# Kernel tuning notes

Measured on AMD Instinct MI355X. Metric: run time of the kernel, lower is better.

The kernel has to match this reference:

```python
import jax, jax.numpy as jnp
import numpy as np

N = 256

def _dct_mat(n):
    # orthonormal DCT-II matrix: (D @ v) == scipy.fftpack.dct(v, norm='ortho')
    k = np.arange(n)[:, None]
    i = np.arange(n)[None, :]
    D = np.cos(np.pi * (2 * i + 1) * k / (2 * n)) * np.sqrt(2.0 / n)
    D[0] *= np.sqrt(0.5)
    return jnp.asarray(D, jnp.float32)

DCT = _dct_mat(N)

def conv3(x, w, b):
    y = jax.lax.conv_general_dilated(x, w, (1, 1), [(1, 1), (1, 1)],
                                     dimension_numbers=('NCHW', 'OIHW', 'NCHW'))
    return y + b[None, :, None, None]

def bn(x, g, b, m, v):
    inv = jax.lax.rsqrt(v + 1e-5)
    return (x - m[None, :, None, None]) * (inv * g)[None, :, None, None] + b[None, :, None, None]

def pool2(x):
    B, C, H, W = x.shape
    return x.reshape(B, C, H // 2, 2, W // 2, 2).mean(axis=(3, 5))


def setup_inputs() -> dict:
    key = jax.random.key(0)
    ks = jax.random.split(key, 32)
    B = 16
    d = {}
    d['x'] = jax.random.normal(ks[0], (B, 3, N, N), jnp.float32)
    d['dct_mean'] = jax.random.normal(ks[1], (3, N, N), jnp.float32) * 0.1
    d['dct_std'] = jnp.abs(jax.random.normal(ks[2], (3, N, N), jnp.float32)) + 0.5
    d['w_spa'] = jax.random.normal(ks[3], (32, 3, 3, 3), jnp.float32) * 0.1
    d['b_spa'] = jnp.zeros((32,), jnp.float32)
    d['w_fre'] = jax.random.normal(ks[4], (32, 3, 3, 3), jnp.float32) * 0.1
    d['b_fre'] = jnp.zeros((32,), jnp.float32)
    d['bn0_g'] = jnp.abs(jax.random.normal(ks[5], (64,), jnp.float32)) + 0.5
    d['bn0_b'] = jax.random.normal(ks[6], (64,), jnp.float32) * 0.1
    d['bn0_m'] = jax.random.normal(ks[7], (64,), jnp.float32) * 0.1
    d['bn0_v'] = jax.random.uniform(ks[8], (64,), jnp.float32) + 0.5
    d['cls_w1'] = jax.random.normal(ks[9], (32, 64, 3, 3), jnp.float32) * 0.05
    d['cls_b1'] = jnp.zeros((32,), jnp.float32)
    d['cls_w'] = jax.random.normal(ks[10], (9, 32, 32, 3, 3), jnp.float32) * 0.05
    d['cls_b'] = jnp.zeros((9, 32), jnp.float32)
    d['cbn_g'] = jnp.abs(jax.random.normal(ks[11], (10, 32), jnp.float32)) + 0.5
    d['cbn_b'] = jax.random.normal(ks[12], (10, 32), jnp.float32) * 0.1
    d['cbn_m'] = jax.random.normal(ks[13], (10, 32), jnp.float32) * 0.1
    d['cbn_v'] = jax.random.uniform(ks[14], (10, 32), jnp.float32) + 0.5
    d['fc_w'] = jax.random.normal(ks[15], (2, 32), jnp.float32) * 0.1
    d['fc_b'] = jnp.zeros((2,), jnp.float32)
    return d


def reference(x, dct_mean, dct_std, w_spa, b_spa, w_fre, b_fre,
              bn0_g, bn0_b, bn0_m, bn0_v,
              cls_w1, cls_b1, cls_w, cls_b,
              cbn_g, cbn_b, cbn_m, cbn_v, fc_w, fc_b):
    # DCT branch: torch code detaches x before DCT
    xd = jax.lax.stop_gradient(x)
    # dct2: DCT along last axis then second-to-last -> D @ X @ D^T
    xf = jnp.einsum('ij,bcjk,lk->bcil', DCT, xd, DCT)
    xf = jnp.log(jnp.abs(xf) + 1e-13)
    xf = (xf - dct_mean[None]) / dct_std[None]

    fs = conv3(x, w_spa, b_spa)
    ff = conv3(xf, w_fre, b_fre)
    feat = jnp.concatenate([fs, ff], axis=1)  # [B,64,256,256]
    feature_map = jax.nn.relu(bn(feat, bn0_g, bn0_b, bn0_m, bn0_v))

    # classifier: 10 conv-BN-ReLU layers, avg-pool after layers 4, 6, 8
    h = jax.nn.relu(bn(conv3(feature_map, cls_w1, cls_b1),
                       cbn_g[0], cbn_b[0], cbn_m[0], cbn_v[0]))
    for i in range(9):  # layers 2..10
        h = jax.nn.relu(bn(conv3(h, cls_w[i], cls_b[i]),
                           cbn_g[i + 1], cbn_b[i + 1], cbn_m[i + 1], cbn_v[i + 1]))
        if i in (2, 4, 6):  # after overall layer 4, 6, 8
            h = pool2(h)
    h = h.mean(axis=(2, 3))  # adaptive avg pool to 1x1 + flatten -> [B,32]
    logits = h @ fc_w.T + fc_b
    return logits, feature_map
```

## Files before the change

kernel.cpp:

```cpp
#include <hip/hip_runtime.h>
#include <hip/hip_bf16.h>
#include <math.h>

typedef __hip_bfloat16 bf16;
typedef __attribute__((ext_vector_type(8))) short short8;
typedef __attribute__((ext_vector_type(4))) float f32x4;

__device__ __forceinline__ float b2f(short s) {
  unsigned u = ((unsigned)(unsigned short)s) << 16;
  return __builtin_bit_cast(float, u);
}
__device__ __forceinline__ short f2b(float f) {
  bf16 h = __float2bfloat16(f);
  return *reinterpret_cast<short*>(&h);
}

__global__ void k_build_dct(float* __restrict__ D) {
  int k = blockIdx.x, i = threadIdx.x;
  double v = cos(3.14159265358979323846 * (2.0 * i + 1.0) * (double)k / 512.0) *
             0.08838834764831845;
  if (k == 0) v *= 0.7071067811865476;
  D[k * 256 + i] = (float)v;
}

__global__ void k_pack_w(const float* __restrict__ w1,
                         const float* __restrict__ wc, short* __restrict__ wp) {
  int set = blockIdx.x;
  const float* w;
  int C, cbase;
  if (set < 2) {
    w = w1;
    C = 64;
    cbase = set * 32;
  } else {
    w = wc + (set - 2) * 9216;
    C = 32;
    cbase = 0;
  }
  for (int d = threadIdx.x; d < 9216; d += 256) {
    int k = d & 7, l = (d >> 3) & 63, ct = (d >> 9) & 1, tap = d >> 10;
    int co = ct * 16 + (l & 15), cin = (l >> 4) * 8 + k;
    wp[set * 9216 + d] = f2b(w[(co * C + cbase + cin) * 9 + tap]);
  }
}

__global__ __launch_bounds__(256) void k_dct1(const float* __restrict__ D,
                                              const float* __restrict__ x,
                                              float* __restrict__ M1) {
  __shared__ __align__(16) float As[32][84];
  __shared__ __align__(16) float Bs[32][80];
  int tid = threadIdx.x;
  int tx = tid & 15, ty = tid >> 4;
  int k0 = blockIdx.x * 64, i0 = blockIdx.y * 64;
  size_t base = (size_t)blockIdx.z * 65536;
  float acc[4][4];
#pragma unroll
  for (int a = 0; a < 4; ++a)
#pragma unroll
    for (int c = 0; c < 4; ++c) acc[a][c] = 0.f;
  for (int kk = 0; kk < 256; kk += 32) {
    __syncthreads();
#pragma unroll
    for (int s = 0; s < 2; ++s) {
      int idx = s * 256 + tid;
      int i = idx >> 3, k4 = (idx & 7) * 4;
      f32x4 d4 = *(const f32x4*)&D[(i0 + i) * 256 + kk + k4];
#pragma unroll
      for (int q = 0; q < 4; ++q) As[k4 + q][i] = d4[q];
      int j = idx >> 4, c4 = (idx & 15) * 4;
      *(f32x4*)&Bs[j][c4] =
          *(const f32x4*)&x[base + (size_t)(kk + j) * 256 + k0 + c4];
    }
    __syncthreads();
#pragma unroll
    for (int k = 0; k < 32; ++k) {
      f32x4 a4 = *(const f32x4*)&As[k][ty * 4];
      f32x4 b4 = *(const f32x4*)&Bs[k][tx * 4];
#pragma unroll
      for (int ii = 0; ii < 4; ++ii)
#pragma unroll
        for (int jj = 0; jj < 4; ++jj)
          acc[ii][jj] = fmaf(a4[ii], b4[jj], acc[ii][jj]);
    }
  }
#pragma unroll
  for (int ii = 0; ii < 4; ++ii) {
    f32x4 o = {acc[ii][0], acc[ii][1], acc[ii][2], acc[ii][3]};
    *(f32x4*)&M1[base + (size_t)(i0 + ty * 4 + ii) * 256 + k0 + tx * 4] = o;
  }
}

__global__ __launch_bounds__(256) void k_dct2(const float* __restrict__ M1,
                                              const float* __restrict__ D,
                                              const float* __restrict__ dmean,
                                              const float* __restrict__ dstd,
                                              float* __restrict__ xf) {
  __shared__ __align__(16) float As[32][84];
  __shared__ __align__(16) float Bs[32][84];
  int tid = threadIdx.x;
  int tx = tid & 15, ty = tid >> 4;
  int l0 = blockIdx.x * 64, i0 = blockIdx.y * 64;
  int bc = blockIdx.z;
  size_t base = (size_t)bc * 65536;
  int ch = bc % 3;
  float acc[4][4];
#pragma unroll
  for (int a = 0; a < 4; ++a)
#pragma unroll
    for (int c = 0; c < 4; ++c) acc[a][c] = 0.f;
  for (int kk = 0; kk < 256; kk += 32) {
    __syncthreads();
#pragma unroll
    for (int s = 0; s < 2; ++s) {
      int idx = s * 256 + tid;
      int i = idx >> 3, k4 = (idx & 7) * 4;
      f32x4 a4 = *(const f32x4*)&M1[base + (size_t)(i0 + i) * 256 + kk + k4];
      f32x4 b4 = *(const f32x4*)&D[(l0 + i) * 256 + kk + k4];
#pragma unroll
      for (int q = 0; q < 4; ++q) {
        As[k4 + q][i] = a4[q];
        Bs[k4 + q][i] = b4[q];
      }
    }
    __syncthreads();
#pragma unroll
    for (int k = 0; k < 32; ++k) {
      f32x4 a4 = *(const f32x4*)&As[k][ty * 4];
      f32x4 b4 = *(const f32x4*)&Bs[k][tx * 4];
#pragma unroll
      for (int ii = 0; ii < 4; ++ii)
#pragma unroll
        for (int jj = 0; jj < 4; ++jj)
          acc[ii][jj] = fmaf(a4[ii], b4[jj], acc[ii][jj]);
    }
  }
#pragma unroll
  for (int ii = 0; ii < 4; ++ii) {
    int ig = i0 + ty * 4 + ii;
    int ll = l0 + tx * 4;
    int mi = (ch * 256 + ig) * 256 + ll;
    f32x4 dm = *(const f32x4*)&dmean[mi];
    f32x4 ds = *(const f32x4*)&dstd[mi];
    f32x4 o;
#pragma unroll
    for (int jj = 0; jj < 4; ++jj)
      o[jj] = (logf(fabsf(acc[ii][jj]) + 1e-13f) - dm[jj]) / ds[jj];
    *(f32x4*)&xf[base + (size_t)ig * 256 + ll] = o;
  }
}

__global__ __launch_bounds__(256) void k_front_n(
    const float* __restrict__ x, const float* __restrict__ xf,
    const float* __restrict__ w_spa, const float* __restrict__ b_spa,
    const float* __restrict__ w_fre, const float* __restrict__ b_fre,
    const float* __restrict__ g, const float* __restrict__ bb,
    const float* __restrict__ m, const float* __restrict__ vv,
    short* __restrict__ featN0, short* __restrict__ featN1,
    float* __restrict__ feat) {
  __shared__ __align__(16) float xin[3 * 4 * 264];
  __shared__ __align__(16) short fstage[2 * 256 * 32];
  __shared__ float wl[864];
  __shared__ float sc[32], sh[32];
  int z = blockIdx.z;
  const float* in = z ? xf : x;
  const float* w = z ? w_fre : w_spa;
  const float* bias = z ? b_fre : b_spa;
  int tid = threadIdx.x;
  int b = blockIdx.y;
  int y0 = blockIdx.x * 2;
  for (int i = tid; i < 864; i += 256) wl[i] = w[i];
  if (tid < 32) {
    int cgl = z * 32 + tid;
    float s = g[cgl] * rsqrtf(vv[cgl] + 1e-5f);
    sc[tid] = s;
    sh[tid] = (bias[tid] - m[cgl]) * s + bb[cgl];
  }
  const float* inb = in + (size_t)b * 3 * 65536;
  for (int i = tid; i < 792; i += 256) {
    int ci = i / 264, rem = i - ci * 264;
    int r = rem / 66, c = rem - r * 66;
    int gy = y0 - 1 + r;
    f32x4 v = {0.f, 0.f, 0.f, 0.f};
    if ((unsigned)gy < 256u && c >= 1 && c <= 64)
      v = *(const f32x4*)&inb[((size_t)ci << 16) + (gy << 8) + (c * 4 - 4)];
    *(f32x4*)&xin[(ci * 4 + r) * 264 + c * 4] = v;
  }
  __syncthreads();
  int xq = tid & 63, cg = tid >> 6;
  int x0 = xq * 4;
  float acc[2][4][8];
#pragma unroll
  for (int r = 0; r < 2; ++r)
#pragma unroll
    for (int p = 0; p < 4; ++p)
#pragma unroll
      for (int co = 0; co < 8; ++co) acc[r][p][co] = 0.f;
  for (int ci = 0; ci < 3; ++ci) {
    float v[4][6];
#pragma unroll
    for (int r = 0; r < 4; ++r) {
      const float* row = &xin[(ci * 4 + r) * 264];
      f32x4 qA = *(const f32x4*)&row[x0];
      f32x4 qB = *(const f32x4*)&row[x0 + 4];
      f32x4 qC = *(const f32x4*)&row[x0 + 8];
      v[r][0] = qA[3];
      v[r][1] = qB[0];
      v[r][2] = qB[1];
      v[r][3] = qB[2];
      v[r][4] = qB[3];
      v[r][5] = qC[0];
    }
#pragma unroll
    for (int co = 0; co < 8; ++co) {
      int cob = cg * 8 + co;
      float w9[9];
#pragma unroll
      for (int t = 0; t < 9; ++t) w9[t] = wl[cob * 27 + ci * 9 + t];
#pragma unroll
      for (int ky = 0; ky < 3; ++ky)
#pragma unroll
        for (int kx = 0; kx < 3; ++kx) {
          float wv = w9[ky * 3 + kx];
#pragma unroll
          for (int r = 0; r < 2; ++r)
#pragma unroll
            for (int p = 0; p < 4; ++p)
              acc[r][p][co] = fmaf(v[r + ky][p + kx], wv, acc[r][p][co]);
        }
    }
  }
#pragma unroll
  for (int r = 0; r < 2; ++r) {
#pragma unroll
    for (int p = 0; p < 4; ++p) {
      short8 s8;
#pragma unroll
      for (int co = 0; co < 8; ++co) {
        float val = acc[r][p][co] * sc[cg * 8 + co] + sh[cg * 8 + co];
        val = val > 0.f ? val : 0.f;
        acc[r][p][co] = val;
        s8[co] = f2b(val);
      }
      int scg = cg ^ p ^ (xq & 3);
      *(short8*)&fstage[((r * 256 + x0 + p) << 5) + (scg << 3)] = s8;
    }
#pragma unroll
    for (int co = 0; co < 8; ++co) {
      f32x4 o = {acc[r][0][co], acc[r][1][co], acc[r][2][co], acc[r][3][co]};
      f32x4* dst = (f32x4*)&feat[(((size_t)(b * 64 + z * 32 + cg * 8 + co))
                                  << 16) +
                                 ((y0 + r) << 8) + x0];
      __builtin_nontemporal_store(o, dst);
    }
  }
  __syncthreads();
  short* fp = z ? featN1 : featN0;
  size_t rowbase = ((size_t)(b * 256 + y0) * 256) << 5;
#pragma unroll
  for (int k = 0; k < 8; ++k) {
    int c = k * 256 + tid;
    int p2 = (c >> 2) & 255;
    int r = c >> 10;
    int cgc = c & 3;
    int scg = cgc ^ (p2 & 3) ^ ((p2 >> 2) & 3);
    short8 v = *(short8*)&fstage[((r * 256 + p2) << 5) + (scg << 3)];
    *(short8*)(fp + rowbase + (size_t)c * 8) = v;
  }
}

template <int TX, int NP, int YB, bool POOL, bool GW>
__global__ __launch_bounds__(256) void k_conv4(
    const short* __restrict__ in0, const short* __restrict__ in1,
    const float* __restrict__ w, const short* __restrict__ wp,
    const float* __restrict__ bias, const float* __restrict__ g,
    const float* __restrict__ bb, const float* __restrict__ m,
    const float* __restrict__ vv, short* __restrict__ out, int H) {
  constexpr int XT = TX + 2;
  constexpr int NR = (TX == 64) ? YB : 2;
  constexpr int YR = ((TX == 64) ? YB : 4) + 2;
  __shared__ short tile[YR * XT * 32];
  __shared__ short wlds[GW ? 1 : 9216];
  __shared__ float sc[32], sh[32];
  int tid = threadIdx.x;
  int lane = tid & 63, wid = tid >> 6;
  int W = H;
  int b = blockIdx.z, y0 = blockIdx.y * ((TX == 64) ? YB : 4),
      x0 = blockIdx.x * TX;
  if (tid < 32) {
    float s = g[tid] * rsqrtf(vv[tid] + 1e-5f);
    sc[tid] = s;
    sh[tid] = (bias[tid] - m[tid]) * s + bb[tid];
  }
  int px = lane & 15, g4 = lane >> 4;
  int RB = (TX == 64) ? 0 : (wid >> 1) * 2;
  int wx = (TX == 64) ? wid : (wid & 1);
  f32x4 acc[NR][2];
#pragma unroll
  for (int r = 0; r < NR; ++r)
#pragma unroll
    for (int ct = 0; ct < 2; ++ct) acc[r][ct] = {0.f, 0.f, 0.f, 0.f};

  for (int cb = 0; cb < NP; ++cb) {
    if (cb) __syncthreads();
    if constexpr (!GW) {
      for (int d = tid; d < 9216; d += 256) {
        int k = d & 7, l = (d >> 3) & 63, ct = (d >> 9) & 1, tap = d >> 10;
        int co = ct * 16 + (l & 15), cin = (l >> 4) * 8 + k;
        wlds[d] = f2b(w[(co * (NP * 32) + cb * 32 + cin) * 9 + tap]);
      }
    }
    const short* in = cb ? in1 : in0;
    for (int i = tid; i < YR * XT * 4; i += 256) {
      int ir = i / (XT * 4), rem = i - ir * (XT * 4);
      int xl = rem >> 2, cg = rem & 3;
      int gy = y0 - 1 + ir, gx = x0 - 1 + xl;
      short8 v = {0, 0, 0, 0, 0, 0, 0, 0};
      if ((unsigned)gy < (unsigned)H && (unsigned)gx < (unsigned)W)
        v = *(const short8*)(in + (((size_t)(b * H + gy) * W + gx) << 5) + cg * 8);
      *(short8*)&tile[(ir * XT + xl) * 32 +
                      ((cg ^ (xl & 3) ^ ((xl >> 2) & 3)) << 3)] = v;
    }
    __syncthreads();
    short8 wf[9][2];
#pragma unroll
    for (int tap = 0; tap < 9; ++tap)
#pragma unroll
      for (int ct = 0; ct < 2; ++ct) {
        if constexpr (GW)
          wf[tap][ct] = *(const short8*)(wp + cb * 9216 +
                                         ((((tap * 2 + ct) << 6) + lane) << 3));
        else
          wf[tap][ct] = *(short8*)&wlds[(((tap * 2 + ct) << 6) + lane) << 3];
      }
#pragma unroll
    for (int dx = 0; dx < 3; ++dx) {
      int xl = wx * 16 + px + dx;
      int cs = (g4 ^ (xl & 3) ^ ((xl >> 2) & 3)) << 3;
      short8 fr[NR + 2];
#pragma unroll
      for (int ir = 0; ir < NR + 2; ++ir)
        fr[ir] = *(short8*)&tile[((RB + ir) * XT + xl) * 32 + cs];
#pragma unroll
      for (int dy = 0; dy < 3; ++dy)
#pragma unroll
        for (int r = 0; r < NR; ++r)
#pragma unroll
          for (int ct = 0; ct < 2; ++ct)
            acc[r][ct] = __builtin_amdgcn_mfma_f32_16x16x32_bf16(
                wf[dy * 3 + dx][ct], fr[r + dy], acc[r][ct], 0, 0, 0);
    }
  }
  int xg = x0 + wx * 16 + px;
  if constexpr (POOL) {
    int H2 = H >> 1;
#pragma unroll
    for (int pr = 0; pr < NR / 2; ++pr) {
#pragma unroll
      for (int ct = 0; ct < 2; ++ct) {
        unsigned short u[4];
#pragma unroll
        for (int q = 0; q < 4; ++q) {
          int co = ct * 16 + g4 * 4 + q;
          float v0 = acc[2 * pr][ct][q] * sc[co] + sh[co];
          float v1 = acc[2 * pr + 1][ct][q] * sc[co] + sh[co];
          v0 = v0 > 0.f ? v0 : 0.f;
          v1 = v1 > 0.f ? v1 : 0.f;
          float s2 = v0 + v1;
          float o = s2 + __shfl_xor(s2, 1, 64);
          u[q] = (unsigned short)f2b(0.25f * o);
        }
        if (!(px & 1)) {
          uint2 pk;
          pk.x = (unsigned)u[0] | ((unsigned)u[1] << 16);
          pk.y = (unsigned)u[2] | ((unsigned)u[3] << 16);
          int row = (y0 + RB + 2 * pr) >> 1;
          size_t ob = (((size_t)(b * H2 + row) * H2 + (xg >> 1)) << 5) +
                      ct * 16 + g4 * 4;
          *(uint2*)(out + ob) = pk;
        }
      }
    }
  } else {
#pragma unroll
    for (int r = 0; r < NR; ++r) {
      int y = y0 + RB + r;
      size_t ob = (((size_t)(b * H + y) * W + xg) << 5);
#pragma unroll
      for (int ct = 0; ct < 2; ++ct) {
        unsigned short u[4];
#pragma unroll
        for (int q = 0; q < 4; ++q) {
          int co = ct * 16 + g4 * 4 + q;
          float val = acc[r][ct][q] * sc[co] + sh[co];
          val = val > 0.f ? val : 0.f;
          u[q] = (unsigned short)f2b(val);
        }
        uint2 pk;
        pk.x = (unsigned)u[0] | ((unsigned)u[1] << 16);
        pk.y = (unsigned)u[2] | ((unsigned)u[3] << 16);
        *(uint2*)(out + ob + ct * 16 + g4 * 4) = pk;
      }
    }
  }
}

__global__ __launch_bounds__(256) void k_conv_front(
    const float* __restrict__ x, const float* __restrict__ xf,
    const float* __restrict__ w_spa, const float* __restrict__ b_spa,
    const float* __restrict__ w_fre, const float* __restrict__ b_fre,
    const float* __restrict__ g, const float* __restrict__ bb,
    const float* __restrict__ m, const float* __restrict__ vv,
    float* __restrict__ feat) {
  int z = blockIdx.z;
  const float* in = z ? xf : x;
  const float* w = z ? w_fre : w_spa;
  const float* bias = z ? b_fre : b_spa;
  __shared__ float wl[864];
  __shared__ float sc[32], sh[32];
  int tid = threadIdx.x;
  for (int i = tid; i < 864; i += 256) wl[i] = w[i];
  if (tid < 32) {
    int cg = z * 32 + tid;
    float s = g[cg] * rsqrtf(vv[cg] + 1e-5f);
    sc[tid] = s;
    sh[tid] = (bias[tid] - m[cg]) * s + bb[cg];
  }
  __syncthreads();
  int b = blockIdx.y;
  int idx = blockIdx.x * 256 + tid;
  int ry = idx >> 8;
  int xx = idx & 255;
  int y0 = ry * 2;
  const float* inb = in + (size_t)b * 3 * 65536;
  float a0[32], a1[32];
#pragma unroll
  for (int co = 0; co < 32; ++co) {
    a0[co] = 0.f;
    a1[co] = 0.f;
  }
  for (int ci = 0; ci < 3; ++ci) {
    const float* p = inb + (size_t)ci * 65536;
    float v[4][3];
#pragma unroll
    for (int r = 0; r < 4; ++r) {
      int iy = y0 + r - 1;
      bool yok = (unsigned)iy < 256u;
#pragma unroll
      for (int c = 0; c < 3; ++c) {
        int ix = xx + c - 1;
        v[r][c] = (yok && (unsigned)ix < 256u) ? p[iy * 256 + ix] : 0.f;
      }
    }
#pragma unroll
    for (int t9 = 0; t9 < 9; ++t9) {
      int ky = t9 / 3, kx = t9 % 3;
      float v0 = v[ky][kx], v1 = v[ky + 1][kx];
#pragma unroll
      for (int co = 0; co < 32; ++co) {
        float wv = wl[co * 27 + ci * 9 + t9];
        a0[co] = fmaf(v0, wv, a0[co]);
        a1[co] = fmaf(v1, wv, a1[co]);
      }
    }
  }
#pragma unroll
  for (int co = 0; co < 32; ++co) {
    size_t o = ((size_t)(b * 64 + z * 32 + co) * 256 + y0) * 256 + xx;
    float r0 = a0[co] * sc[co] + sh[co];
    float r1 = a1[co] * sc[co] + sh[co];
    feat[o] = r0 > 0.f ? r0 : 0.f;
    feat[o + 256] = r1 > 0.f ? r1 : 0.f;
  }
}

__global__ __launch_bounds__(256) void k_conv1_mfma(
    const float* __restrict__ in, const float* __restrict__ w,
    const float* __restrict__ bias, const float* __restrict__ g,
    const float* __restrict__ bb, const float* __restrict__ m,
    const float* __restrict__ vv, short* __restrict__ out) {
  constexpr int TX = 64, XT = 66;
  __shared__ short tile[4 * XT * 64];
  __shared__ short wlds[9216];
  __shared__ float sc[32], sh[32];
  int tid = threadIdx.x;
  int lane = tid & 63, wid = tid >> 6;
  int b = blockIdx.z, y0 = blockIdx.y * 2, x0 = blockIdx.x * TX;
  if (tid < 32) {
    float s = g[tid] * rsqrtf(vv[tid] + 1e-5f);
    sc[tid] = s;
    sh[tid] = (bias[tid] - m[tid]) * s + bb[tid];
  }
  for (int ir = 0; ir < 4; ++ir) {
    int gy = y0 - 1 + ir;
    bool yok = (unsigned)gy < 256u;
    for (int ch = tid; ch < XT * 8; ch += 256) {
      int xl = ch >> 3, cg = ch & 7;
      int gx = x0 - 1 + xl;
      short8 v = {0, 0, 0, 0, 0, 0, 0, 0};
      if (yok && (unsigned)gx < 256u) {
        const float* p = in + (((size_t)(b * 64 + cg * 8)) << 16) + (gy << 8) + gx;
#pragma unroll
        for (int k = 0; k < 8; ++k) v[k] = f2b(p[(size_t)k << 16]);
      }
      *(short8*)&tile[((ir * XT + xl) << 6) + ((cg ^ (xl & 7)) << 3)] = v;
    }
  }
  int px = lane & 15, g4 = lane >> 4;
  int wx = wid;
  f32x4 acc[2][2];
#pragma unroll
  for (int r = 0; r < 2; ++r)
#pragma unroll
    for (int ct = 0; ct < 2; ++ct) acc[r][ct] = {0.f, 0.f, 0.f, 0.f};
  for (int cb = 0; cb < 2; ++cb) {
    __syncthreads();
    for (int d = tid; d < 9216; d += 256) {
      int k = d & 7, l = (d >> 3) & 63, ct = (d >> 9) & 1, tap = d >> 10;
      int co = ct * 16 + (l & 15), cin = (l >> 4) * 8 + k;
      wlds[d] = f2b(w[(co * 64 + cb * 32 + cin) * 9 + tap]);
    }
    __syncthreads();
    short8 wf[9][2];
#pragma unroll
    for (int tap = 0; tap < 9; ++tap)
#pragma unroll
      for (int ct = 0; ct < 2; ++ct)
        wf[tap][ct] = *(short8*)&wlds[(((tap * 2 + ct) << 6) + lane) << 3];
#pragma unroll
    for (int dx = 0; dx < 3; ++dx) {
      short8 fr[4];
#pragma unroll
      for (int ir = 0; ir < 4; ++ir) {
        int xl = wx * 16 + px + dx;
        fr[ir] = *(short8*)&tile[((ir * XT + xl) << 6) +
                                 (((cb * 4 + g4) ^ (xl & 7)) << 3)];
      }
#pragma unroll
      for (int dy = 0; dy < 3; ++dy)
#pragma unroll
        for (int r = 0; r < 2; ++r)
#pragma unroll
          for (int ct = 0; ct < 2; ++ct)
            acc[r][ct] = __builtin_amdgcn_mfma_f32_16x16x32_bf16(
                wf[dy * 3 + dx][ct], fr[r + dy], acc[r][ct], 0, 0, 0);
    }
  }
#pragma unroll
  for (int r = 0; r < 2; ++r) {
    int y = y0 + r;
    int xg = x0 + wx * 16 + px;
    size_t ob = (((size_t)(b * 256 + y) * 256 + xg) << 5);
#pragma unroll
    for (int ct = 0; ct < 2; ++ct) {
      unsigned short u[4];
#pragma unroll
      for (int q = 0; q < 4; ++q) {
        int co = ct * 16 + g4 * 4 + q;
        float val = acc[r][ct][q] * sc[co] + sh[co];
        val = val > 0.f ? val : 0.f;
        u[q] = (unsigned short)f2b(val);
      }
      uint2 pk;
      pk.x = (unsigned)u[0] | ((unsigned)u[1] << 16);
      pk.y = (unsigned)u[2] | ((unsigned)u[3] << 16);
      *(uint2*)(out + ob + ct * 16 + g4 * 4) = pk;
    }
  }
}

__global__ __launch_bounds__(256) void k_tail(
    const short* __restrict__ in, const float* __restrict__ w9,
    const float* __restrict__ b9, const float* __restrict__ w10,
    const float* __restrict__ b10, const float* __restrict__ cg9,
    const float* __restrict__ cb9, const float* __restrict__ cm9,
    const float* __restrict__ cv9, const float* __restrict__ cg10,
    const float* __restrict__ cb10, const float* __restrict__ cm10,
    const float* __restrict__ cv10, const float* __restrict__ fw,
    const float* __restrict__ fb, float* __restrict__ logits) {
  __shared__ short tileA[32768];
  __shared__ short tileB[32768];
  __shared__ short wlds[9216];
  __shared__ float sc[2][32], sh[2][32];
  __shared__ float red[16][8];
  __shared__ float smean[32];
  int tid = threadIdx.x;
  int lane = tid & 63, wv = tid >> 6;
  int b = blockIdx.x;
  int px = lane & 15, g4 = lane >> 4;

  if (tid < 64) {
    int l = tid >> 5, c = tid & 31;
    const float* g = l ? cg10 : cg9;
    const float* bb = l ? cb10 : cb9;
    const float* m = l ? cm10 : cm9;
    const float* v = l ? cv10 : cv9;
    const float* bi = l ? b10 : b9;
    float s = g[c] * rsqrtf(v[c] + 1e-5f);
    sc[l][c] = s;
    sh[l][c] = (bi[c] - m[c]) * s + bb[c];
  }
  const short* src = in + (size_t)b * 32768;
  for (int i = tid; i < 4096; i += 256) {
    int p = i >> 2, cg = i & 3;
    int xc = p & 31;
    short8 v = *(const short8*)(src + p * 32 + cg * 8);
    *(short8*)&tileA[p * 32 + ((cg ^ (xc & 3) ^ ((xc >> 2) & 3)) << 3)] = v;
  }
  float psum[2][4];
#pragma unroll
  for (int ct = 0; ct < 2; ++ct)
#pragma unroll
    for (int q = 0; q < 4; ++q) psum[ct][q] = 0.f;

  for (int layer = 0; layer < 2; ++layer) {
    if (layer) __syncthreads();
    const float* w = layer ? w10 : w9;
    for (int d = tid; d < 9216; d += 256) {
      int k = d & 7, l = (d >> 3) & 63, ct = (d >> 9) & 1, tap = d >> 10;
      int co = ct * 16 + (l & 15), cin = (l >> 4) * 8 + k;
      wlds[d] = f2b(w[(co * 32 + cin) * 9 + tap]);
    }
    __syncthreads();
    short8 wf[9][2];
#pragma unroll
    for (int tap = 0; tap < 9; ++tap)
#pragma unroll
      for (int ct = 0; ct < 2; ++ct)
        wf[tap][ct] = *(short8*)&wlds[(((tap * 2 + ct) << 6) + lane) << 3];
    const short* ts = layer ? tileB : tileA;
    for (int u = wv; u < 16; u += 4) {
      int rw = u >> 1, cw = u & 1;
      f32x4 acc[4][2];
#pragma unroll
      for (int r = 0; r < 4; ++r)
#pragma unroll
        for (int ct = 0; ct < 2; ++ct) acc[r][ct] = {0.f, 0.f, 0.f, 0.f};
#pragma unroll
      for (int dx = 0; dx < 3; ++dx) {
        int gx = cw * 16 + px + dx - 1;
        bool xok = (unsigned)gx < 32u;
        int cs = (g4 ^ (gx & 3) ^ ((gx >> 2) & 3)) << 3;
        short8 fr[6];
        short8 zz = {0, 0, 0, 0, 0, 0, 0, 0};
#pragma unroll
        for (int ir = 0; ir < 6; ++ir) {
          int gy = rw * 4 + ir - 1;
          fr[ir] = (xok && (unsigned)gy < 32u)
                       ? *(const short8*)&ts[(gy * 32 + gx) * 32 + cs]
                       : zz;
        }
#pragma unroll
        for (int dy = 0; dy < 3; ++dy)
#pragma unroll
          for (int r = 0; r < 4; ++r)
#pragma unroll
            for (int ct = 0; ct < 2; ++ct)
              acc[r][ct] = __builtin_amdgcn_mfma_f32_16x16x32_bf16(
                  wf[dy * 3 + dx][ct], fr[r + dy], acc[r][ct], 0, 0, 0);
      }
      int xc = cw * 16 + px;
#pragma unroll
      for (int r = 0; r < 4; ++r) {
        int y = rw * 4 + r;
#pragma unroll
        for (int ct = 0; ct < 2; ++ct) {
          float v4[4];
#pragma unroll
          for (int q = 0; q < 4; ++q) {
            int co = ct * 16 + g4 * 4 + q;
            float val = acc[r][ct][q] * sc[layer][co] + sh[layer][co];
            v4[q] = val > 0.f ? val : 0.f;
          }
          if (layer == 0) {
            int cg = ct * 2 + (g4 >> 1);
            int scg = cg ^ (xc & 3) ^ ((xc >> 2) & 3);
            uint2 pk;
            pk.x = (unsigned)(unsigned short)f2b(v4[0]) |
                   ((unsigned)(unsigned short)f2b(v4[1]) << 16);
            pk.y = (unsigned)(unsigned short)f2b(v4[2]) |
                   ((unsigned)(unsigned short)f2b(v4[3]) << 16);
            *(uint2*)&tileB[(y * 32 + xc) * 32 + (scg << 3) + (g4 & 1) * 4] = pk;
          } else {
#pragma unroll
            for (int q = 0; q < 4; ++q) psum[ct][q] += v4[q];
          }
        }
      }
    }
  }
#pragma unroll
  for (int o = 1; o < 16; o <<= 1)
#pragma unroll
    for (int ct = 0; ct < 2; ++ct)
#pragma unroll
      for (int q = 0; q < 4; ++q)
        psum[ct][q] += __shfl_xor(psum[ct][q], o, 64);
  if (px == 0) {
#pragma unroll
    for (int ct = 0; ct < 2; ++ct)
#pragma unroll
      for (int q = 0; q < 4; ++q) red[wv * 4 + g4][ct * 4 + q] = psum[ct][q];
  }
  __syncthreads();
  if (tid < 32) {
    int ct = tid >> 4, g4r = (tid >> 2) & 3, q = tid & 3;
    float s = red[g4r][ct * 4 + q] + red[4 + g4r][ct * 4 + q] +
              red[8 + g4r][ct * 4 + q] + red[12 + g4r][ct * 4 + q];
    smean[tid] = s * (1.f / 1024.f);
  }
  __syncthreads();
  if (tid < 2) {
    float s = fb[tid];
    for (int c = 0; c < 32; ++c) s = fmaf(smean[c], fw[tid * 32 + c], s);
    logits[b * 2 + tid] = s;
  }
}

extern "C" void kernel_launch(void* const* d_in, const int* in_sizes, int n_in,
                              void* d_out, int out_size, void* d_ws,
                              size_t ws_size, hipStream_t stream) {
  const float* x = (const float*)d_in[0];
  const float* dmean = (const float*)d_in[1];
  const float* dstd = (const float*)d_in[2];
  const float* w_spa = (const float*)d_in[3];
  const float* b_spa = (const float*)d_in[4];
  const float* w_fre = (const float*)d_in[5];
  const float* b_fre = (const float*)d_in[6];
  const float* bn0_g = (const float*)d_in[7];
  const float* bn0_b = (const float*)d_in[8];
  const float* bn0_m = (const float*)d_in[9];
  const float* bn0_v = (const float*)d_in[10];
  const float* cls_w1 = (const float*)d_in[11];
  const float* cls_b1 = (const float*)d_in[12];
  const float* cls_w = (const float*)d_in[13];
  const float* cls_b = (const float*)d_in[14];
  const float* cbn_g = (const float*)d_in[15];
  const float* cbn_b = (const float*)d_in[16];
  const float* cbn_m = (const float*)d_in[17];
  const float* cbn_v = (const float*)d_in[18];
  const float* fc_w = (const float*)d_in[19];
  const float* fc_b = (const float*)d_in[20];

  float* out = (float*)d_out;
  float* logits = out;
  float* feat = out + 32;

  char* ws = (char*)d_ws;
  const size_t MB = 1048576ull;
  bool bigws = ws_size >= 193ull * MB;

  short *bufA, *bufB, *featN0 = nullptr, *featN1 = nullptr, *wpack = nullptr;
  float *D, *M1, *xf;
  if (bigws) {
    featN0 = (short*)ws;
    featN1 = (short*)(ws + 64 * MB);
    bufA = (short*)(ws + 128 * MB);
    bufB = (short*)ws;
    wpack = (short*)(ws + 192 * MB);
    D = (float*)(ws + 128 * MB);
    M1 = (float*)(ws + 129 * MB);
    xf = (float*)(ws + 144 * MB);
  } else {
    bufA = (short*)ws;
    bufB = (short*)(ws + 64 * MB);
    D = (float*)ws;
    M1 = (float*)(ws + 1 * MB);
    xf = (float*)(ws + 64 * MB);
  }

  k_build_dct<<<dim3(256), dim3(256), 0, stream>>>(D);
  if (bigws) k_pack_w<<<dim3(9), dim3(256), 0, stream>>>(cls_w1, cls_w, wpack);
  k_dct1<<<dim3(4, 4, 48), dim3(256), 0, stream>>>(D, x, M1);
  k_dct2<<<dim3(4, 4, 48), dim3(256), 0, stream>>>(M1, D, dmean, dstd, xf);

  const int WS = 32 * 32 * 9;
  if (bigws) {
    k_front_n<<<dim3(128, 16, 2), dim3(256), 0, stream>>>(
        x, xf, w_spa, b_spa, w_fre, b_fre, bn0_g, bn0_b, bn0_m, bn0_v, featN0,
        featN1, feat);
    k_conv4<64, 2, 8, false, true><<<dim3(4, 32, 16), dim3(256), 0, stream>>>(
        featN0, featN1, nullptr, wpack, cls_b1, cbn_g, cbn_b, cbn_m, cbn_v,
        bufA, 256);
    k_conv4<64, 1, 8, false, true><<<dim3(4, 32, 16), dim3(256), 0, stream>>>(
        bufA, nullptr, nullptr, wpack + 2 * 9216, cls_b + 0 * 32, cbn_g + 32,
        cbn_b + 32, cbn_m + 32, cbn_v + 32, bufB, 256);
    k_conv4<64, 1, 8, false, true><<<dim3(4, 32, 16), dim3(256), 0, stream>>>(
        bufB, nullptr, nullptr, wpack + 3 * 9216, cls_b + 1 * 32, cbn_g + 64,
        cbn_b + 64, cbn_m + 64, cbn_v + 64, bufA, 256);
    k_conv4<64, 1, 8, true, true><<<dim3(4, 32, 16), dim3(256), 0, stream>>>(
        bufA, nullptr, nullptr, wpack + 4 * 9216, cls_b + 2 * 32, cbn_g + 96,
        cbn_b + 96, cbn_m + 96, cbn_v + 96, bufB, 256);
    k_conv4<64, 1, 8, false, true><<<dim3(2, 16, 16), dim3(256), 0, stream>>>(
        bufB, nullptr, nullptr, wpack + 5 * 9216, cls_b + 3 * 32, cbn_g + 128,
        cbn_b + 128, cbn_m + 128, cbn_v + 128, bufA, 128);
    k_conv4<64, 1, 8, true, true><<<dim3(2, 16, 16), dim3(256), 0, stream>>>(
        bufA, nullptr, nullptr, wpack + 6 * 9216, cls_b + 4 * 32, cbn_g + 160,
        cbn_b + 160, cbn_m + 160, cbn_v + 160, bufB, 128);
    k_conv4<32, 1, 4, false, true><<<dim3(2, 16, 16), dim3(256), 0, stream>>>(
        bufB, nullptr, nullptr, wpack + 7 * 9216, cls_b + 5 * 32, cbn_g + 192,
        cbn_b + 192, cbn_m + 192, cbn_v + 192, bufA, 64);
    k_conv4<32, 1, 4, true, true><<<dim3(2, 16, 16), dim3(256), 0, stream>>>(
        bufA, nullptr, nullptr, wpack + 8 * 9216, cls_b + 6 * 32, cbn_g + 224,
        cbn_b + 224, cbn_m + 224, cbn_v + 224, bufB, 64);
  } else {
    k_conv_front<<<dim3(128, 16, 2), dim3(256), 0, stream>>>(
        x, xf, w_spa, b_spa, w_fre, b_fre, bn0_g, bn0_b, bn0_m, bn0_v, feat);
    k_conv1_mfma<<<dim3(4, 128, 16), dim3(256), 0, stream>>>(
        feat, cls_w1, cls_b1, cbn_g, cbn_b, cbn_m, cbn_v, bufA);
    k_conv4<64, 1, 8, false, false><<<dim3(4, 32, 16), dim3(256), 0, stream>>>(
        bufA, nullptr, cls_w + 0 * WS, nullptr, cls_b + 0 * 32, cbn_g + 32,
        cbn_b + 32, cbn_m + 32, cbn_v + 32, bufB, 256);
    k_conv4<64, 1, 8, false, false><<<dim3(4, 32, 16), dim3(256), 0, stream>>>(
        bufB, nullptr, cls_w + 1 * WS, nullptr, cls_b + 1 * 32, cbn_g + 64,
        cbn_b + 64, cbn_m + 64, cbn_v + 64, bufA, 256);
    k_conv4<64, 1, 8, true, false><<<dim3(4, 32, 16), dim3(256), 0, stream>>>(
        bufA, nullptr, cls_w + 2 * WS, nullptr, cls_b + 2 * 32, cbn_g + 96,
        cbn_b + 96, cbn_m + 96, cbn_v + 96, bufB, 256);
    k_conv4<64, 1, 8, false, false><<<dim3(2, 16, 16), dim3(256), 0, stream>>>(
        bufB, nullptr, cls_w + 3 * WS, nullptr, cls_b + 3 * 32, cbn_g + 128,
        cbn_b + 128, cbn_m + 128, cbn_v + 128, bufA, 128);
    k_conv4<64, 1, 8, true, false><<<dim3(2, 16, 16), dim3(256), 0, stream>>>(
        bufA, nullptr, cls_w + 4 * WS, nullptr, cls_b + 4 * 32, cbn_g + 160,
        cbn_b + 160, cbn_m + 160, cbn_v + 160, bufB, 128);
    k_conv4<32, 1, 4, false, false><<<dim3(2, 16, 16), dim3(256), 0, stream>>>(
        bufB, nullptr, cls_w + 5 * WS, nullptr, cls_b + 5 * 32, cbn_g + 192,
        cbn_b + 192, cbn_m + 192, cbn_v + 192, bufA, 64);
    k_conv4<32, 1, 4, true, false><<<dim3(2, 16, 16), dim3(256), 0, stream>>>(
        bufA, nullptr, cls_w + 6 * WS, nullptr, cls_b + 6 * 32, cbn_g + 224,
        cbn_b + 224, cbn_m + 224, cbn_v + 224, bufB, 64);
  }

  k_tail<<<dim3(16), dim3(256), 0, stream>>>(
      bufB, cls_w + 7 * WS, cls_b + 7 * 32, cls_w + 8 * WS, cls_b + 8 * 32,
      cbn_g + 256, cbn_b + 256, cbn_m + 256, cbn_v + 256, cbn_g + 288,
      cbn_b + 288, cbn_m + 288, cbn_v + 288, fc_w, fc_b, logits);
}
```

Measured before the change: 399.1 us.

## Store intermediate classifier activations as fp8 e4m3 to halve memory traffic

Intermediate NHWC activation buffers between the conv layers are now stored as fp8 e4m3 instead of bf16. Each kernel dequantizes to bf16 when staging into shared memory, so the MFMA math is unchanged. This halves global read and write traffic for the memory-bound conv chain and shrinks the workspace layout. The cost is extra per-element conversion ALU work and reduced activation precision, which may hurt accuracy of the logits.

```diff
diff --git a/kernel.cpp b/kernel.cpp
--- a/kernel.cpp
+++ b/kernel.cpp
@@ -1,8 +1,10 @@
 #include <hip/hip_runtime.h>
 #include <hip/hip_bf16.h>
+#include <hip/hip_fp8.h>
 #include <math.h>
 
 typedef __hip_bfloat16 bf16;
+typedef unsigned char uchar;
 typedef __attribute__((ext_vector_type(8))) short short8;
 typedef __attribute__((ext_vector_type(4))) float f32x4;
 
@@ -13,6 +15,19 @@
 __device__ __forceinline__ short f2b(float f) {
   bf16 h = __float2bfloat16(f);
   return *reinterpret_cast<short*>(&h);
+}
+__device__ __forceinline__ uchar f2q(float f) {
+  __hip_fp8_e4m3 t(f);
+  return (uchar)t.__x;
+}
+__device__ __forceinline__ float q2f(uchar c) {
+  __hip_fp8_e4m3 t;
+  t.__x = (__hip_fp8_storage_t)c;
+  return (float)t;
+}
+__device__ __forceinline__ unsigned pk4q(float a, float b, float c, float d) {
+  return (unsigned)f2q(a) | ((unsigned)f2q(b) << 8) | ((unsigned)f2q(c) << 16) |
+         ((unsigned)f2q(d) << 24);
 }
 
 __global__ void k_build_dct(float* __restrict__ D) {
@@ -155,7 +170,7 @@
     const float* __restrict__ w_fre, const float* __restrict__ b_fre,
     const float* __restrict__ g, const float* __restrict__ bb,
     const float* __restrict__ m, const float* __restrict__ vv,
-    short* __restrict__ featN0, short* __restrict__ featN1,
+    uchar* __restrict__ featN0, uchar* __restrict__ featN1,
     float* __restrict__ feat) {
   __shared__ __align__(16) float xin[3 * 4 * 264];
   __shared__ __align__(16) short fstage[2 * 256 * 32];
@@ -254,8 +269,8 @@
     }
   }
   __syncthreads();
-  short* fp = z ? featN1 : featN0;
-  size_t rowbase = ((size_t)(b * 256 + y0) * 256) << 5;
+  uchar* fp = z ? featN1 : featN0;
+  size_t rowbase = ((size_t)(b * 256 + y0) * 256) * 32;
 #pragma unroll
   for (int k = 0; k < 8; ++k) {
     int c = k * 256 + tid;
@@ -264,17 +279,20 @@
     int cgc = c & 3;
     int scg = cgc ^ (p2 & 3) ^ ((p2 >> 2) & 3);
     short8 v = *(short8*)&fstage[((r * 256 + p2) << 5) + (scg << 3)];
-    *(short8*)(fp + rowbase + (size_t)c * 8) = v;
-  }
-}
-
-template <int TX, int NP, int YB, bool POOL, bool GW>
+    uint2 pk2;
+    pk2.x = pk4q(b2f(v[0]), b2f(v[1]), b2f(v[2]), b2f(v[3]));
+    pk2.y = pk4q(b2f(v[4]), b2f(v[5]), b2f(v[6]), b2f(v[7]));
+    *(uint2*)(fp + rowbase + (size_t)c * 8) = pk2;
+  }
+}
+
+template <int TX, int NP, int YB, bool POOL, bool GW, bool F8>
 __global__ __launch_bounds__(256) void k_conv4(
-    const short* __restrict__ in0, const short* __restrict__ in1,
+    const void* __restrict__ in0, const void* __restrict__ in1,
     const float* __restrict__ w, const short* __restrict__ wp,
     const float* __restrict__ bias, const float* __restrict__ g,
     const float* __restrict__ bb, const float* __restrict__ m,
-    const float* __restrict__ vv, short* __restrict__ out, int H) {
+    const float* __restrict__ vv, void* __restrict__ out, int H) {
   constexpr int XT = TX + 2;
   constexpr int NR = (TX == 64) ? YB : 2;
   constexpr int YR = ((TX == 64) ? YB : 4) + 2;
@@ -309,16 +327,41 @@
         wlds[d] = f2b(w[(co * (NP * 32) + cb * 32 + cin) * 9 + tap]);
       }
     }
-    const short* in = cb ? in1 : in0;
-    for (int i = tid; i < YR * XT * 4; i += 256) {
-      int ir = i / (XT * 4), rem = i - ir * (XT * 4);
-      int xl = rem >> 2, cg = rem & 3;
-      int gy = y0 - 1 + ir, gx = x0 - 1 + xl;
-      short8 v = {0, 0, 0, 0, 0, 0, 0, 0};
-      if ((unsigned)gy < (unsigned)H && (unsigned)gx < (unsigned)W)
-        v = *(const short8*)(in + (((size_t)(b * H + gy) * W + gx) << 5) + cg * 8);
-      *(short8*)&tile[(ir * XT + xl) * 32 +
-                      ((cg ^ (xl & 3) ^ ((xl >> 2) & 3)) << 3)] = v;
+    const void* in = cb ? in1 : in0;
+    if constexpr (F8) {
+      const uchar* inq = (const uchar*)in;
+      for (int i = tid; i < YR * XT * 2; i += 256) {
+        int ir = i / (XT * 2), rem = i - ir * (XT * 2);
+        int xl = rem >> 1, c2 = rem & 1;
+        int gy = y0 - 1 + ir, gx = x0 - 1 + xl;
+        short8 raw = {0, 0, 0, 0, 0, 0, 0, 0};
+        if ((unsigned)gy < (unsigned)H && (unsigned)gx < (unsigned)W)
+          raw = *(const short8*)(inq + ((size_t)(b * H + gy) * W + gx) * 32 +
+                                 c2 * 16);
+        const uchar* pb = (const uchar*)&raw;
+        short8 o0, o1;
+#pragma unroll
+        for (int k = 0; k < 8; ++k) {
+          o0[k] = f2b(q2f(pb[k]));
+          o1[k] = f2b(q2f(pb[k + 8]));
+        }
+        int sw = (xl & 3) ^ ((xl >> 2) & 3);
+        *(short8*)&tile[(ir * XT + xl) * 32 + (((c2 * 2) ^ sw) << 3)] = o0;
+        *(short8*)&tile[(ir * XT + xl) * 32 + (((c2 * 2 + 1) ^ sw) << 3)] = o1;
+      }
+    } else {
+      const short* ins = (const short*)in;
+      for (int i = tid; i < YR * XT * 4; i += 256) {
+        int ir = i / (XT * 4), rem = i - ir * (XT * 4);
+        int xl = rem >> 2, cg = rem & 3;
+        int gy = y0 - 1 + ir, gx = x0 - 1 + xl;
+        short8 v = {0, 0, 0, 0, 0, 0, 0, 0};
+        if ((unsigned)gy < (unsigned)H && (unsigned)gx < (unsigned)W)
+          v = *(const short8*)(ins + (((size_t)(b * H + gy) * W + gx) << 5) +
+                               cg * 8);
+        *(short8*)&tile[(ir * XT + xl) * 32 +
+                        ((cg ^ (xl & 3) ^ ((xl >> 2) & 3)) << 3)] = v;
+      }
     }
     __syncthreads();
     short8 wf[9][2];
@@ -357,7 +400,7 @@
     for (int pr = 0; pr < NR / 2; ++pr) {
 #pragma unroll
       for (int ct = 0; ct < 2; ++ct) {
-        unsigned short u[4];
+        float o4[4];
 #pragma unroll
         for (int q = 0; q < 4; ++q) {
           int co = ct * 16 + g4 * 4 + q;
@@ -366,17 +409,25 @@
           v0 = v0 > 0.f ? v0 : 0.f;
           v1 = v1 > 0.f ? v1 : 0.f;
           float s2 = v0 + v1;
-          float o = s2 + __shfl_xor(s2, 1, 64);
-          u[q] = (unsigned short)f2b(0.25f * o);
+          o4[q] = 0.25f * (s2 + __shfl_xor(s2, 1, 64));
         }
         if (!(px & 1)) {
-          uint2 pk;
-          pk.x = (unsigned)u[0] | ((unsigned)u[1] << 16);
-          pk.y = (unsigned)u[2] | ((unsigned)u[3] << 16);
           int row = (y0 + RB + 2 * pr) >> 1;
-          size_t ob = (((size_t)(b * H2 + row) * H2 + (xg >> 1)) << 5) +
-                      ct * 16 + g4 * 4;
-          *(uint2*)(out + ob) = pk;
+          if constexpr (F8) {
+            unsigned pk = pk4q(o4[0], o4[1], o4[2], o4[3]);
+            size_t ob = ((size_t)(b * H2 + row) * H2 + (xg >> 1)) * 32 +
+                        ct * 16 + g4 * 4;
+            *(unsigned*)((uchar*)out + ob) = pk;
+          } else {
+            uint2 pk;
+            pk.x = (unsigned)(unsigned short)f2b(o4[0]) |
+                   ((unsigned)(unsigned short)f2b(o4[1]) << 16);
+            pk.y = (unsigned)(unsigned short)f2b(o4[2]) |
+                   ((unsigned)(unsigned short)f2b(o4[3]) << 16);
+            size_t ob = (((size_t)(b * H2 + row) * H2 + (xg >> 1)) << 5) +
+                        ct * 16 + g4 * 4;
+            *(uint2*)((short*)out + ob) = pk;
+          }
         }
       }
     }
@@ -384,21 +435,28 @@
 #pragma unroll
     for (int r = 0; r < NR; ++r) {
       int y = y0 + RB + r;
-      size_t ob = (((size_t)(b * H + y) * W + xg) << 5);
 #pragma unroll
       for (int ct = 0; ct < 2; ++ct) {
-        unsigned short u[4];
+        float o4[4];
 #pragma unroll
         for (int q = 0; q < 4; ++q) {
           int co = ct * 16 + g4 * 4 + q;
           float val = acc[r][ct][q] * sc[co] + sh[co];
-          val = val > 0.f ? val : 0.f;
-          u[q] = (unsigned short)f2b(val);
+          o4[q] = val > 0.f ? val : 0.f;
         }
-        uint2 pk;
-        pk.x = (unsigned)u[0] | ((unsigned)u[1] << 16);
-        pk.y = (unsigned)u[2] | ((unsigned)u[3] << 16);
-        *(uint2*)(out + ob + ct * 16 + g4 * 4) = pk;
+        if constexpr (F8) {
+          unsigned pk = pk4q(o4[0], o4[1], o4[2], o4[3]);
+          size_t ob = ((size_t)(b * H + y) * W + xg) * 32 + ct * 16 + g4 * 4;
+          *(unsigned*)((uchar*)out + ob) = pk;
+        } else {
+          uint2 pk;
+          pk.x = (unsigned)(unsigned short)f2b(o4[0]) |
+                 ((unsigned)(unsigned short)f2b(o4[1]) << 16);
+          pk.y = (unsigned)(unsigned short)f2b(o4[2]) |
+                 ((unsigned)(unsigned short)f2b(o4[3]) << 16);
+          size_t ob = (((size_t)(b * H + y) * W + xg) << 5) + ct * 16 + g4 * 4;
+          *(uint2*)((short*)out + ob) = pk;
+        }
       }
     }
   }
@@ -568,8 +626,9 @@
   }
 }
 
+template <bool F8>
 __global__ __launch_bounds__(256) void k_tail(
-    const short* __restrict__ in, const float* __restrict__ w9,
+    const void* __restrict__ in, const float* __restrict__ w9,
     const float* __restrict__ b9, const float* __restrict__ w10,
     const float* __restrict__ b10, const float* __restrict__ cg9,
     const float* __restrict__ cb9, const float* __restrict__ cm9,
@@ -599,12 +658,30 @@
     sc[l][c] = s;
     sh[l][c] = (bi[c] - m[c]) * s + bb[c];
   }
-  const short* src = in + (size_t)b * 32768;
-  for (int i = tid; i < 4096; i += 256) {
-    int p = i >> 2, cg = i & 3;
-    int xc = p & 31;
-    short8 v = *(const short8*)(src + p * 32 + cg * 8);
-    *(short8*)&tileA[p * 32 + ((cg ^ (xc & 3) ^ ((xc >> 2) & 3)) << 3)] = v;
+  if constexpr (F8) {
+    const uchar* src = (const uchar*)in + (size_t)b * 32768;
+    for (int i = tid; i < 2048; i += 256) {
+      int p = i >> 1, c2 = i & 1, xc = p & 31;
+      short8 raw = *(const short8*)(src + p * 32 + c2 * 16);
+      const uchar* pb = (const uchar*)&raw;
+      short8 o0, o1;
+#pragma unroll
+      for (int k = 0; k < 8; ++k) {
+        o0[k] = f2b(q2f(pb[k]));
+        o1[k] = f2b(q2f(pb[k + 8]));
+      }
+      int sw = (xc & 3) ^ ((xc >> 2) & 3);
+      *(short8*)&tileA[p * 32 + (((c2 * 2) ^ sw) << 3)] = o0;
+      *(short8*)&tileA[p * 32 + (((c2 * 2 + 1) ^ sw) << 3)] = o1;
+    }
+  } else {
+    const short* src = (const short*)in + (size_t)b * 32768;
+    for (int i = tid; i < 4096; i += 256) {
+      int p = i >> 2, cg = i & 3;
+      int xc = p & 31;
+      short8 v = *(const short8*)(src + p * 32 + cg * 8);
+      *(short8*)&tileA[p * 32 + ((cg ^ (xc & 3) ^ ((xc >> 2) & 3)) << 3)] = v;
+    }
   }
   float psum[2][4];
 #pragma unroll
@@ -749,89 +826,106 @@
   const size_t MB = 1048576ull;
   bool bigws = ws_size >= 193ull * MB;
 
-  short *bufA, *bufB, *featN0 = nullptr, *featN1 = nullptr, *wpack = nullptr;
-  float *D, *M1, *xf;
-  if (bigws) {
-    featN0 = (short*)ws;
-    featN1 = (short*)(ws + 64 * MB);
-    bufA = (short*)(ws + 128 * MB);
-    bufB = (short*)ws;
-    wpack = (short*)(ws + 192 * MB);
-    D = (float*)(ws + 128 * MB);
-    M1 = (float*)(ws + 129 * MB);
-    xf = (float*)(ws + 144 * MB);
-  } else {
-    bufA = (short*)ws;
-    bufB = (short*)(ws + 64 * MB);
-    D = (float*)ws;
-    M1 = (float*)(ws + 1 * MB);
-    xf = (float*)(ws + 64 * MB);
-  }
-
-  k_build_dct<<<dim3(256), dim3(256), 0, stream>>>(D);
-  if (bigws) k_pack_w<<<dim3(9), dim3(256), 0, stream>>>(cls_w1, cls_w, wpack);
-  k_dct1<<<dim3(4, 4, 48), dim3(256), 0, stream>>>(D, x, M1);
-  k_dct2<<<dim3(4, 4, 48), dim3(256), 0, stream>>>(M1, D, dmean, dstd, xf);
-
   const int WS = 32 * 32 * 9;
   if (bigws) {
+    uchar* featN0 = (uchar*)ws;
+    uchar* featN1 = (uchar*)(ws + 32 * MB);
+    uchar* bufA = (uchar*)(ws + 64 * MB);
+    uchar* bufB = (uchar*)ws;
+    short* wpack = (short*)(ws + 192 * MB);
+    float* D = (float*)(ws + 96 * MB);
+    float* M1 = (float*)(ws + 97 * MB);
+    float* xf = (float*)(ws + 112 * MB);
+
+    k_build_dct<<<dim3(256), dim3(256), 0, stream>>>(D);
+    k_pack_w<<<dim3(9), dim3(256), 0, stream>>>(cls_w1, cls_w, wpack);
+    k_dct1<<<dim3(4, 4, 48), dim3(256), 0, stream>>>(D, x, M1);
+    k_dct2<<<dim3(4, 4, 48), dim3(256), 0, stream>>>(M1, D, dmean, dstd, xf);
+
     k_front_n<<<dim3(128, 16, 2), dim3(256), 0, stream>>>(
         x, xf, w_spa, b_spa, w_fre, b_fre, bn0_g, bn0_b, bn0_m, bn0_v, featN0,
         featN1, feat);
-    k_conv4<64, 2, 8, false, true><<<dim3(4, 32, 16), dim3(256), 0, stream>>>(
-        featN0, featN1, nullptr, wpack, cls_b1, cbn_g, cbn_b, cbn_m, cbn_v,
-        bufA, 256);
-    k_conv4<64, 1, 8, false, true><<<dim3(4, 32, 16), dim3(256), 0, stream>>>(
-        bufA, nullptr, nullptr, wpack + 2 * 9216, cls_b + 0 * 32, cbn_g + 32,
-        cbn_b + 32, cbn_m + 32, cbn_v + 32, bufB, 256);
-    k_conv4<64, 1, 8, false, true><<<dim3(4, 32, 16), dim3(256), 0, stream>>>(
-        bufB, nullptr, nullptr, wpack + 3 * 9216, cls_b + 1 * 32, cbn_g + 64,
-        cbn_b + 64, cbn_m + 64, cbn_v + 64, bufA, 256);
-    k_conv4<64, 1, 8, true, true><<<dim3(4, 32, 16), dim3(256), 0, stream>>>(
-        bufA, nullptr, nullptr, wpack + 4 * 9216, cls_b + 2 * 32, cbn_g + 96,
-        cbn_b + 96, cbn_m + 96, cbn_v + 96, bufB, 256);
-    k_conv4<64, 1, 8, false, true><<<dim3(2, 16, 16), dim3(256), 0, stream>>>(
-        bufB, nullptr, nullptr, wpack + 5 * 9216, cls_b + 3 * 32, cbn_g + 128,
-        cbn_b + 128, cbn_m + 128, cbn_v + 128, bufA, 128);
-    k_conv4<64, 1, 8, true, true><<<dim3(2, 16, 16), dim3(256), 0, stream>>>(
-        bufA, nullptr, nullptr, wpack + 6 * 9216, cls_b + 4 * 32, cbn_g + 160,
-        cbn_b + 160, cbn_m + 160, cbn_v + 160, bufB, 128);
-    k_conv4<32, 1, 4, false, true><<<dim3(2, 16, 16), dim3(256), 0, stream>>>(
-        bufB, nullptr, nullptr, wpack + 7 * 9216, cls_b + 5 * 32, cbn_g + 192,
-        cbn_b + 192, cbn_m + 192, cbn_v + 192, bufA, 64);
-    k_conv4<32, 1, 4, true, true><<<dim3(2, 16, 16), dim3(256), 0, stream>>>(
-        bufA, nullptr, nullptr, wpack + 8 * 9216, cls_b + 6 * 32, cbn_g + 224,
-        cbn_b + 224, cbn_m + 224, cbn_v + 224, bufB, 64);
+    k_conv4<64, 2, 8, false, true, true>
+        <<<dim3(4, 32, 16), dim3(256), 0, stream>>>(
+            featN0, featN1, nullptr, wpack, cls_b1, cbn_g, cbn_b, cbn_m, cbn_v,
+            bufA, 256);
+    k_conv4<64, 1, 8, false, true, true>
+        <<<dim3(4, 32, 16), dim3(256), 0, stream>>>(
+            bufA, nullptr, nullptr, wpack + 2 * 9216, cls_b + 0 * 32,
+            cbn_g + 32, cbn_b + 32, cbn_m + 32, cbn_v + 32, bufB, 256);
+    k_conv4<64, 1, 8, false, true, true>
+        <<<dim3(4, 32, 16), dim3(256), 0, stream>>>(
+            bufB, nullptr, nullptr, wpack + 3 * 9216, cls_b + 1 * 32,
+            cbn_g + 64, cbn_b + 64, cbn_m + 64, cbn_v + 64, bufA, 256);
+    k_conv4<64, 1, 8, true, true, true>
+        <<<dim3(4, 32, 16), dim3(256), 0, stream>>>(
+            bufA, nullptr, nullptr, wpack + 4 * 9216, cls_b + 2 * 32,
+            cbn_g + 96, cbn_b + 96, cbn_m + 96, cbn_v + 96, bufB, 256);
+    k_conv4<64, 1, 8, false, true, true>
+        <<<dim3(2, 16, 16), dim3(256), 0, stream>>>(
+            bufB, nullptr, nullptr, wpack + 5 * 9216, cls_b + 3 * 32,
+            cbn_g + 128, cbn_b + 128, cbn_m + 128, cbn_v + 128, bufA, 128);
+    k_conv4<64, 1, 8, true, true, true>
+        <<<dim3(2, 16, 16), dim3(256), 0, stream>>>(
+            bufA, nullptr, nullptr, wpack + 6 * 9216, cls_b + 4 * 32,
+            cbn_g + 160, cbn_b + 160, cbn_m + 160, cbn_v + 160, bufB, 128);
+    k_conv4<32, 1, 4, false, true, true>
+        <<<dim3(2, 16, 16), dim3(256), 0, stream>>>(
+            bufB, nullptr, nullptr, wpack + 7 * 9216, cls_b + 5 * 32,
+            cbn_g + 192, cbn_b + 192, cbn_m + 192, cbn_v + 192, bufA, 64);
+    k_conv4<32, 1, 4, true, true, true>
+        <<<dim3(2, 16, 16), dim3(256), 0, stream>>>(
+            bufA, nullptr, nullptr, wpack + 8 * 9216, cls_b + 6 * 32,
+            cbn_g + 224, cbn_b + 224, cbn_m + 224, cbn_v + 224, bufB, 64);
+    k_tail<true><<<dim3(16), dim3(256), 0, stream>>>(
+        bufB, cls_w + 7 * WS, cls_b + 7 * 32, cls_w + 8 * WS, cls_b + 8 * 32,
+        cbn_g + 256, cbn_b + 256, cbn_m + 256, cbn_v + 256, cbn_g + 288,
+        cbn_b + 288, cbn_m + 288, cbn_v + 288, fc_w, fc_b, logits);
   } else {
+    short* bufA = (short*)ws;
+    short* bufB = (short*)(ws + 64 * MB);
+    float* D = (float*)ws;
+    float* M1 = (float*)(ws + 1 * MB);
+    float* xf = (float*)(ws + 64 * MB);
+
+    k_build_dct<<<dim3(256), dim3(256), 0, stream>>>(D);
+    k_dct1<<<dim3(4, 4, 48), dim3(256), 0, stream>>>(D, x, M1);
+    k_dct2<<<dim3(4, 4, 48), dim3(256), 0, stream>>>(M1, D, dmean, dstd, xf);
     k_conv_front<<<dim3(128, 16, 2), dim3(256), 0, stream>>>(
         x, xf, w_spa, b_spa, w_fre, b_fre, bn0_g, bn0_b, bn0_m, bn0_v, feat);
     k_conv1_mfma<<<dim3(4, 128, 16), dim3(256), 0, stream>>>(
         feat, cls_w1, cls_b1, cbn_g, cbn_b, cbn_m, cbn_v, bufA);
-    k_conv4<64, 1, 8, false, false><<<dim3(4, 32, 16), dim3(256), 0, stream>>>(
-        bufA, nullptr, cls_w + 0 * WS, nullptr, cls_b + 0 * 32, cbn_g + 32,
-        cbn_b + 32, cbn_m + 32, cbn_v + 32, bufB, 256);
-    k_conv4<64, 1, 8, false, false><<<dim3(4, 32, 16), dim3(256), 0, stream>>>(
-        bufB, nullptr, cls_w + 1 * WS, nullptr, cls_b + 1 * 32, cbn_g + 64,
-        cbn_b + 64, cbn_m + 64, cbn_v + 64, bufA, 256);
-    k_conv4<64, 1, 8, true, false><<<dim3(4, 32, 16), dim3(256), 0, stream>>>(
-        bufA, nullptr, cls_w + 2 * WS, nullptr, cls_b + 2 * 32, cbn_g + 96,
-        cbn_b + 96, cbn_m + 96, cbn_v + 96, bufB, 256);
-    k_conv4<64, 1, 8, false, false><<<dim3(2, 16, 16), dim3(256), 0, stream>>>(
-        bufB, nullptr, cls_w + 3 * WS, nullptr, cls_b + 3 * 32, cbn_g + 128,
-        cbn_b + 128, cbn_m + 128, cbn_v + 128, bufA, 128);
-    k_conv4<64, 1, 8, true, false><<<dim3(2, 16, 16), dim3(256), 0, stream>>>(
-        bufA, nullptr, cls_w + 4 * WS, nullptr, cls_b + 4 * 32, cbn_g + 160,
-        cbn_b + 160, cbn_m + 160, cbn_v + 160, bufB, 128);
-    k_conv4<32, 1, 4, false, false><<<dim3(2, 16, 16), dim3(256), 0, stream>>>(
-        bufB, nullptr, cls_w + 5 * WS, nullptr, cls_b + 5 * 32, cbn_g + 192,
-        cbn_b + 192, cbn_m + 192, cbn_v + 192, bufA, 64);
-    k_conv4<32, 1, 4, true, false><<<dim3(2, 16, 16), dim3(256), 0, stream>>>(
-        bufA, nullptr, cls_w + 6 * WS, nullptr, cls_b + 6 * 32, cbn_g + 224,
-        cbn_b + 224, cbn_m + 224, cbn_v + 224, bufB, 64);
-  }
-
-  k_tail<<<dim3(16), dim3(256), 0, stream>>>(
-      bufB, cls_w + 7 * WS, cls_b + 7 * 32, cls_w + 8 * WS, cls_b + 8 * 32,
-      cbn_g + 256, cbn_b + 256, cbn_m + 256, cbn_v + 256, cbn_g + 288,
-      cbn_b + 288, cbn_m + 288, cbn_v + 288, fc_w, fc_b, logits);
-}
+    k_conv4<64, 1, 8, false, false, false>
+        <<<dim3(4, 32, 16), dim3(256), 0, stream>>>(
+            bufA, nullptr, cls_w + 0 * WS, nullptr, cls_b + 0 * 32, cbn_g + 32,
+            cbn_b + 32, cbn_m + 32, cbn_v + 32, bufB, 256);
+    k_conv4<64, 1, 8, false, false, false>
+        <<<dim3(4, 32, 16), dim3(256), 0, stream>>>(
+            bufB, nullptr, cls_w + 1 * WS, nullptr, cls_b + 1 * 32, cbn_g + 64,
+            cbn_b + 64, cbn_m + 64, cbn_v + 64, bufA, 256);
+    k_conv4<64, 1, 8, true, false, false>
+        <<<dim3(4, 32, 16), dim3(256), 0, stream>>>(
+            bufA, nullptr, cls_w + 2 * WS, nullptr, cls_b + 2 * 32, cbn_g + 96,
+            cbn_b + 96, cbn_m + 96, cbn_v + 96, bufB, 256);
+    k_conv4<64, 1, 8, false, false, false>
+        <<<dim3(2, 16, 16), dim3(256), 0, stream>>>(
+            bufB, nullptr, cls_w + 3 * WS, nullptr, cls_b + 3 * 32,
+            cbn_g + 128, cbn_b + 128, cbn_m + 128, cbn_v + 128, bufA, 128);
+    k_conv4<64, 1, 8, true, false, false>
+        <<<dim3(2, 16, 16), dim3(256), 0, stream>>>(
+            bufA, nullptr, cls_w + 4 * WS, nullptr, cls_b + 4 * 32,
+            cbn_g + 160, cbn_b + 160, cbn_m + 160, cbn_v + 160, bufB, 128);
+    k_conv4<32, 1, 4, false, false, false>
+        <<<dim3(2, 16, 16), dim3(256), 0, stream>>>(
+            bufB, nullptr, cls_w + 5 * WS, nullptr, cls_b + 5 * 32,
+            cbn_g + 192, cbn_b + 192, cbn_m + 192, cbn_v + 192, bufA, 64);
+    k_conv4<32, 1, 4, true, false, false>
+        <<<dim3(2, 16, 16), dim3(256), 0, stream>>>(
+            bufA, nullptr, cls_w + 6 * WS, nullptr, cls_b + 6 * 32,
+            cbn_g + 224, cbn_b + 224, cbn_m + 224, cbn_v + 224, bufB, 64);
+    k_tail<false><<<dim3(16), dim3(256), 0, stream>>>(
+        bufB, cls_w + 7 * WS, cls_b + 7 * 32, cls_w + 8 * WS, cls_b + 8 * 32,
+        cbn_g + 256, cbn_b + 256, cbn_m + 256, cbn_v + 256, cbn_g + 288,
+        cbn_b + 288, cbn_m + 288, cbn_v + 288, fc_w, fc_b, logits);
+  }
+}
```

Measured after the change: 365.2 us. -8.5%, faster.
